# Performance work log

Measured on AMD Instinct MI355X. Metric: run time of the kernel, lower is better.

Reference implementation:

```python
import jax, jax.numpy as jnp
import numpy as np

HIDDEN = 768
NUM_EXPERTS = 8
TOP_K = 2
NUM_CLASSES = 191
Z_LOSS_COEF = 0.1
LB_COEF = 0.1
FFN = 4 * HIDDEN
EPS = 1e-5  # torch LayerNorm default


def layer_norm(x, g, b):
    m = jnp.mean(x, axis=-1, keepdims=True)
    v = jnp.mean(jnp.square(x - m), axis=-1, keepdims=True)
    return (x - m) * jax.lax.rsqrt(v + EPS) * g + b


def setup_inputs() -> dict:
    key = jax.random.key(0)
    ks = jax.random.split(key, 12)
    s = 0.02
    B, N = 256, 32
    inp = {
        'trunk_out1': jax.random.normal(ks[0], (B, N, HIDDEN), jnp.float32),
        # router: Linear -> LayerNorm -> ReLU -> (Dropout, eval) -> Linear
        'rw1': jax.random.normal(ks[1], (HIDDEN, HIDDEN), jnp.float32) * s,
        'rb1': jnp.zeros((HIDDEN,), jnp.float32),
        'rlg': jnp.ones((HIDDEN,), jnp.float32),
        'rlb': jnp.zeros((HIDDEN,), jnp.float32),
        'rw2': jax.random.normal(ks[2], (HIDDEN, NUM_EXPERTS), jnp.float32) * s,
        'rb2': jnp.zeros((NUM_EXPERTS,), jnp.float32),
        # stacked expert params [E, ...]
        'ew1': jax.random.normal(ks[3], (NUM_EXPERTS, HIDDEN, FFN), jnp.float32) * s,
        'eb1': jnp.zeros((NUM_EXPERTS, FFN), jnp.float32),
        'el1g': jnp.ones((NUM_EXPERTS, FFN), jnp.float32),
        'el1b': jnp.zeros((NUM_EXPERTS, FFN), jnp.float32),
        'ew2': jax.random.normal(ks[4], (NUM_EXPERTS, FFN, HIDDEN), jnp.float32) * s,
        'eb2': jnp.zeros((NUM_EXPERTS, HIDDEN), jnp.float32),
        'el2g': jnp.ones((NUM_EXPERTS, HIDDEN), jnp.float32),
        'el2b': jnp.zeros((NUM_EXPERTS, HIDDEN), jnp.float32),
        'ew3': jax.random.normal(ks[5], (NUM_EXPERTS, HIDDEN, NUM_CLASSES), jnp.float32) * s,
        'eb3': jnp.zeros((NUM_EXPERTS, NUM_CLASSES), jnp.float32),
    }
    return inp


def reference(trunk_out1, rw1, rb1, rlg, rlb, rw2, rb2,
              ew1, eb1, el1g, el1b, ew2, eb2, el2g, el2b, ew3, eb3):
    B, N, D = trunk_out1.shape
    x = trunk_out1.reshape(-1, D)  # [T, D], T = B*N
    T = x.shape[0]

    # router (dropout is identity in eval)
    h = jax.nn.relu(layer_norm(x @ rw1 + rb1, rlg, rlb))
    logits = h @ rw2 + rb2  # [T, E]
    probs = jax.nn.softmax(logits, axis=-1)

    topk_vals, topk_idx = jax.lax.top_k(probs, TOP_K)
    topk_vals = topk_vals / jnp.sum(topk_vals, axis=-1, keepdims=True)
    rows = jnp.arange(T)[:, None]
    mask = jnp.zeros_like(probs).at[rows, topk_idx].set(topk_vals)  # [T, E]

    z_loss = Z_LOSS_COEF * jnp.mean(jnp.square(jax.nn.logsumexp(logits, axis=-1)))
    load = jnp.mean(mask, axis=0)
    lb_loss = LB_COEF * jnp.sum(jnp.square(load - 1.0 / NUM_EXPERTS))
    aux_loss = z_loss + lb_loss

    # per-expert FFN; weighting by mask (0 for unselected) matches the
    # gather -> FFN -> weighted scatter-add of the original.
    final_logits = jnp.zeros((T, NUM_CLASSES), x.dtype)
    for e in range(NUM_EXPERTS):
        h1 = jax.nn.relu(layer_norm(x @ ew1[e] + eb1[e], el1g, el1b := el1b) if False else layer_norm(x @ ew1[e] + eb1[e], el1g[e], el1b[e]))
        h1 = jax.nn.relu(layer_norm(x @ ew1[e] + eb1[e], el1g[e], el1b[e]))  # [T, 4D]
        h2 = jax.nn.relu(layer_norm(h1 @ ew2[e] + eb2[e], el2g[e], el2b[e]))  # [T, D]
        out_e = h2 @ ew3[e] + eb3[e]  # [T, C]
        final_logits = final_logits + out_e * mask[:, e:e + 1]

    final_logits = final_logits.reshape(B, N, NUM_CLASSES).mean(axis=1)
    return final_logits, aux_loss
```

## Files before the change

### kernel.cpp

```cpp
#include <hip/hip_runtime.h>
#include <hip/hip_bf16.h>
#include <stdint.h>

#define T_TOK   8192
#define D_HID   768
#define NE      8
#define FFN_DIM 3072
#define NCLS    191
#define NSEQ    32
#define NSLOT   (T_TOK * 2)
#define NSLOTP  (NSLOT + 128)
#define LN_EPS  1e-5f
#define OUT_N   (256 * NCLS)

typedef __bf16 bf16x8 __attribute__((ext_vector_type(8)));
typedef float  f32x4  __attribute__((ext_vector_type(4)));

static __device__ __forceinline__ float bf2f(unsigned short u) {
    return __uint_as_float(((unsigned)u) << 16);
}
static __device__ __forceinline__ unsigned short f2bf(float f) {
    return __builtin_bit_cast(unsigned short, (__bf16)f);
}
static __device__ __forceinline__ float bfround(float f) {
    return (float)((__bf16)f);
}

__global__ void k_zero(float* __restrict__ out, unsigned* __restrict__ counts,
                       unsigned* __restrict__ cursors, float* __restrict__ zsum,
                       float* __restrict__ loadsum) {
    int i = blockIdx.x * 256 + threadIdx.x;
    if (i < OUT_N + 1) out[i] = 0.0f;
    if (i < NE) { counts[i] = 0u; cursors[i] = 0u; loadsum[i] = 0.0f; }
    if (i == 0) zsum[0] = 0.0f;
}

__global__ __launch_bounds__(256) void k_prep(
    const float* __restrict__ X, const float* __restrict__ RW1, const float* __restrict__ EW3,
    unsigned short* __restrict__ Xb, unsigned short* __restrict__ RW1h,
    unsigned short* __restrict__ RW1l, unsigned short* __restrict__ W3h,
    unsigned short* __restrict__ W3l) {
    const int bid = blockIdx.x, tid = threadIdx.x;
    if (bid < 3072) {
        size_t i0 = (size_t)bid * 2048 + (size_t)tid * 8;
        float4 a = *reinterpret_cast<const float4*>(X + i0);
        float4 b = *reinterpret_cast<const float4*>(X + i0 + 4);
        unsigned short t[8] = {f2bf(a.x), f2bf(a.y), f2bf(a.z), f2bf(a.w),
                               f2bf(b.x), f2bf(b.y), f2bf(b.z), f2bf(b.w)};
        *reinterpret_cast<uint4*>(Xb + i0) = *reinterpret_cast<uint4*>(t);
        return;
    }
    __shared__ float tile[64][65];
    const int rr = tid >> 2, c4 = (tid & 3) * 16;
    if (bid < 3216) {
        int t = bid - 3072, kt = t / 12, nt = t % 12;
        const float* src = RW1 + (size_t)(kt * 64 + rr) * D_HID + nt * 64 + c4;
        #pragma unroll
        for (int q = 0; q < 4; ++q) {
            float4 v = *reinterpret_cast<const float4*>(src + q * 4);
            tile[rr][c4 + q * 4 + 0] = v.x; tile[rr][c4 + q * 4 + 1] = v.y;
            tile[rr][c4 + q * 4 + 2] = v.z; tile[rr][c4 + q * 4 + 3] = v.w;
        }
        __syncthreads();
        unsigned short th[16], tl[16];
        #pragma unroll
        for (int j = 0; j < 16; ++j) {
            float f = tile[c4 + j][rr];
            th[j] = f2bf(f); tl[j] = f2bf(f - bfround(f));
        }
        size_t o = (size_t)(nt * 64 + rr) * D_HID + kt * 64 + c4;
        *reinterpret_cast<uint4*>(RW1h + o)     = *reinterpret_cast<uint4*>(&th[0]);
        *reinterpret_cast<uint4*>(RW1h + o + 8) = *reinterpret_cast<uint4*>(&th[8]);
        *reinterpret_cast<uint4*>(RW1l + o)     = *reinterpret_cast<uint4*>(&tl[0]);
        *reinterpret_cast<uint4*>(RW1l + o + 8) = *reinterpret_cast<uint4*>(&tl[8]);
    } else {
        int t = bid - 3216, e = t / 36, s = t % 36, kt = s / 3, ct = s % 3;
        const float* src = EW3 + (size_t)e * D_HID * NCLS + (size_t)(kt * 64 + rr) * NCLS;
        #pragma unroll
        for (int j = 0; j < 16; ++j) {
            int c = ct * 64 + c4 + j;
            tile[rr][c4 + j] = (c < NCLS) ? src[c] : 0.0f;
        }
        __syncthreads();
        unsigned short th[16], tl[16];
        #pragma unroll
        for (int j = 0; j < 16; ++j) {
            float f = tile[c4 + j][rr];
            th[j] = f2bf(f); tl[j] = f2bf(f - bfround(f));
        }
        size_t o = (size_t)(e * 192 + ct * 64 + rr) * D_HID + kt * 64 + c4;
        *reinterpret_cast<uint4*>(W3h + o)     = *reinterpret_cast<uint4*>(&th[0]);
        *reinterpret_cast<uint4*>(W3h + o + 8) = *reinterpret_cast<uint4*>(&th[8]);
        *reinterpret_cast<uint4*>(W3l + o)     = *reinterpret_cast<uint4*>(&tl[0]);
        *reinterpret_cast<uint4*>(W3l + o + 8) = *reinterpret_cast<uint4*>(&tl[8]);
    }
}

__global__ __launch_bounds__(256) void k_rgemm(
    const float* __restrict__ X, const unsigned short* __restrict__ RW1h,
    const unsigned short* __restrict__ RW1l, const float* __restrict__ bias,
    float* __restrict__ C) {
    const int bid = blockIdx.x;
    const int lid = (bid & 7) * 48 + (bid >> 3);
    const int m0 = (lid / 6) * 128, n0 = (lid % 6) * 128;
    __shared__ unsigned short Ah[128][40], Al[128][40], Bh[128][40], Bl[128][40];
    const int tid = threadIdx.x;
    const int wv = tid >> 6, ln = tid & 63;
    const int m_off = (wv >> 1) * 64, n_off = (wv & 1) * 64;
    const int lrow = ln & 15, lkg = ln >> 4;
    const int ar = tid >> 1, ac = (tid & 1) * 16;
    const float* aptr = X + (size_t)(m0 + ar) * D_HID + ac;
    const unsigned short* bph = RW1h + (size_t)(n0 + ar) * D_HID + ac;
    const unsigned short* bpl = RW1l + (size_t)(n0 + ar) * D_HID + ac;
    f32x4 acc[4][4] = {};
    for (int k0 = 0; k0 < D_HID; k0 += 32) {
        unsigned short th[16], tl[16];
        #pragma unroll
        for (int q = 0; q < 4; ++q) {
            float4 v = *reinterpret_cast<const float4*>(aptr + k0 + q * 4);
            float fv[4] = {v.x, v.y, v.z, v.w};
            #pragma unroll
            for (int j = 0; j < 4; ++j) {
                th[q * 4 + j] = f2bf(fv[j]);
                tl[q * 4 + j] = f2bf(fv[j] - bfround(fv[j]));
            }
        }
        *reinterpret_cast<uint4*>(&Ah[ar][ac])     = *reinterpret_cast<uint4*>(&th[0]);
        *reinterpret_cast<uint4*>(&Ah[ar][ac + 8]) = *reinterpret_cast<uint4*>(&th[8]);
        *reinterpret_cast<uint4*>(&Al[ar][ac])     = *reinterpret_cast<uint4*>(&tl[0]);
        *reinterpret_cast<uint4*>(&Al[ar][ac + 8]) = *reinterpret_cast<uint4*>(&tl[8]);
        *reinterpret_cast<uint4*>(&Bh[ar][ac])     = *reinterpret_cast<const uint4*>(bph + k0);
        *reinterpret_cast<uint4*>(&Bh[ar][ac + 8]) = *reinterpret_cast<const uint4*>(bph + k0 + 8);
        *reinterpret_cast<uint4*>(&Bl[ar][ac])     = *reinterpret_cast<const uint4*>(bpl + k0);
        *reinterpret_cast<uint4*>(&Bl[ar][ac + 8]) = *reinterpret_cast<const uint4*>(bpl + k0 + 8);
        __syncthreads();
        bf16x8 a_h[4], a_l[4];
        #pragma unroll
        for (int i = 0; i < 4; ++i) {
            a_h[i] = *reinterpret_cast<const bf16x8*>(&Ah[m_off + i * 16 + lrow][lkg * 8]);
            a_l[i] = *reinterpret_cast<const bf16x8*>(&Al[m_off + i * 16 + lrow][lkg * 8]);
        }
        #pragma unroll
        for (int j = 0; j < 4; ++j) {
            bf16x8 b_h = *reinterpret_cast<const bf16x8*>(&Bh[n_off + j * 16 + lrow][lkg * 8]);
            bf16x8 b_l = *reinterpret_cast<const bf16x8*>(&Bl[n_off + j * 16 + lrow][lkg * 8]);
            #pragma unroll
            for (int i = 0; i < 4; ++i) {
                acc[i][j] = __builtin_amdgcn_mfma_f32_16x16x32_bf16(a_h[i], b_h, acc[i][j], 0, 0, 0);
                acc[i][j] = __builtin_amdgcn_mfma_f32_16x16x32_bf16(a_h[i], b_l, acc[i][j], 0, 0, 0);
                acc[i][j] = __builtin_amdgcn_mfma_f32_16x16x32_bf16(a_l[i], b_h, acc[i][j], 0, 0, 0);
            }
        }
        __syncthreads();
    }
    #pragma unroll
    for (int i = 0; i < 4; ++i)
        #pragma unroll
        for (int r = 0; r < 4; ++r) {
            int row = m0 + m_off + i * 16 + lkg * 4 + r;
            float* dst = C + (size_t)row * D_HID;
            #pragma unroll
            for (int j = 0; j < 4; ++j) {
                int c = n0 + n_off + j * 16 + lrow;
                dst[c] = acc[i][j][r] + bias[c];
            }
        }
}

__global__ __launch_bounds__(256) void k_ln768_f32(
    float* __restrict__ Xb, const float* __restrict__ g, const float* __restrict__ b) {
    const int row = blockIdx.x;
    float* x = Xb + (size_t)row * D_HID;
    const int tid = threadIdx.x;
    float v0 = x[tid], v1 = x[tid + 256], v2 = x[tid + 512];
    float s = v0 + v1 + v2, s2 = v0 * v0 + v1 * v1 + v2 * v2;
    __shared__ float rs[4], rs2[4], mv[2];
    #pragma unroll
    for (int o = 32; o > 0; o >>= 1) { s += __shfl_down(s, o); s2 += __shfl_down(s2, o); }
    const int wv = tid >> 6, ln = tid & 63;
    if (ln == 0) { rs[wv] = s; rs2[wv] = s2; }
    __syncthreads();
    if (tid == 0) {
        float ts = rs[0] + rs[1] + rs[2] + rs[3];
        float ts2 = rs2[0] + rs2[1] + rs2[2] + rs2[3];
        float m = ts / D_HID;
        mv[0] = m; mv[1] = rsqrtf(ts2 / D_HID - m * m + LN_EPS);
    }
    __syncthreads();
    float m = mv[0], r = mv[1];
    x[tid]       = fmaxf((v0 - m) * r * g[tid]       + b[tid],       0.f);
    x[tid + 256] = fmaxf((v1 - m) * r * g[tid + 256] + b[tid + 256], 0.f);
    x[tid + 512] = fmaxf((v2 - m) * r * g[tid + 512] + b[tid + 512], 0.f);
}

__global__ __launch_bounds__(256) void k_ln768_bf16(
    unsigned short* __restrict__ Xb, const float* __restrict__ g, const float* __restrict__ b,
    const unsigned* __restrict__ eos, const unsigned* __restrict__ totp) {
    const int row = blockIdx.x;
    if ((unsigned)row >= *totp) return;
    const unsigned e = eos[row];
    const float* gp = g + (size_t)e * D_HID;
    const float* bp = b + (size_t)e * D_HID;
    unsigned short* x = Xb + (size_t)row * D_HID;
    const int tid = threadIdx.x;
    float f[4] = {0.f, 0.f, 0.f, 0.f};
    if (tid < 192) {
        ushort4 u = *reinterpret_cast<const ushort4*>(x + tid * 4);
        f[0] = bf2f(u.x); f[1] = bf2f(u.y); f[2] = bf2f(u.z); f[3] = bf2f(u.w);
    }
    float s = f[0] + f[1] + f[2] + f[3];
    float s2 = f[0] * f[0] + f[1] * f[1] + f[2] * f[2] + f[3] * f[3];
    __shared__ float rs[4], rs2[4], mv[2];
    #pragma unroll
    for (int o = 32; o > 0; o >>= 1) { s += __shfl_down(s, o); s2 += __shfl_down(s2, o); }
    const int wv = tid >> 6, ln = tid & 63;
    if (ln == 0) { rs[wv] = s; rs2[wv] = s2; }
    __syncthreads();
    if (tid == 0) {
        float ts = rs[0] + rs[1] + rs[2] + rs[3];
        float ts2 = rs2[0] + rs2[1] + rs2[2] + rs2[3];
        float m = ts / D_HID;
        mv[0] = m; mv[1] = rsqrtf(ts2 / D_HID - m * m + LN_EPS);
    }
    __syncthreads();
    if (tid < 192) {
        float m = mv[0], r = mv[1];
        float4 gg = *reinterpret_cast<const float4*>(gp + tid * 4);
        float4 bb = *reinterpret_cast<const float4*>(bp + tid * 4);
        ushort4 o;
        o.x = f2bf(fmaxf((f[0] - m) * r * gg.x + bb.x, 0.f));
        o.y = f2bf(fmaxf((f[1] - m) * r * gg.y + bb.y, 0.f));
        o.z = f2bf(fmaxf((f[2] - m) * r * gg.z + bb.z, 0.f));
        o.w = f2bf(fmaxf((f[3] - m) * r * gg.w + bb.w, 0.f));
        *reinterpret_cast<ushort4*>(x + tid * 4) = o;
    }
}

__global__ __launch_bounds__(256) void k_ln3072_bf16(
    unsigned short* __restrict__ Xb, const float* __restrict__ g, const float* __restrict__ b,
    const unsigned* __restrict__ eos, const unsigned* __restrict__ totp) {
    const int row = blockIdx.x;
    if ((unsigned)row >= *totp) return;
    const unsigned e = eos[row];
    const float* gp = g + (size_t)e * FFN_DIM;
    const float* bp = b + (size_t)e * FFN_DIM;
    unsigned short* x = Xb + (size_t)row * FFN_DIM;
    const int tid = threadIdx.x;
    float f[12];
    #pragma unroll
    for (int i = 0; i < 3; ++i) {
        ushort4 u = *reinterpret_cast<const ushort4*>(x + (i * 256 + tid) * 4);
        f[i * 4 + 0] = bf2f(u.x); f[i * 4 + 1] = bf2f(u.y);
        f[i * 4 + 2] = bf2f(u.z); f[i * 4 + 3] = bf2f(u.w);
    }
    float s = 0.f, s2 = 0.f;
    #pragma unroll
    for (int i = 0; i < 12; ++i) { s += f[i]; s2 += f[i] * f[i]; }
    __shared__ float rs[4], rs2[4], mv[2];
    #pragma unroll
    for (int o = 32; o > 0; o >>= 1) { s += __shfl_down(s, o); s2 += __shfl_down(s2, o); }
    const int wv = tid >> 6, ln = tid & 63;
    if (ln == 0) { rs[wv] = s; rs2[wv] = s2; }
    __syncthreads();
    if (tid == 0) {
        float ts = rs[0] + rs[1] + rs[2] + rs[3];
        float ts2 = rs2[0] + rs2[1] + rs2[2] + rs2[3];
        float m = ts / FFN_DIM;
        mv[0] = m; mv[1] = rsqrtf(ts2 / FFN_DIM - m * m + LN_EPS);
    }
    __syncthreads();
    float m = mv[0], r = mv[1];
    #pragma unroll
    for (int i = 0; i < 3; ++i) {
        int off = (i * 256 + tid) * 4;
        float4 gg = *reinterpret_cast<const float4*>(gp + off);
        float4 bb = *reinterpret_cast<const float4*>(bp + off);
        ushort4 o;
        o.x = f2bf(fmaxf((f[i * 4 + 0] - m) * r * gg.x + bb.x, 0.f));
        o.y = f2bf(fmaxf((f[i * 4 + 1] - m) * r * gg.y + bb.y, 0.f));
        o.z = f2bf(fmaxf((f[i * 4 + 2] - m) * r * gg.z + bb.z, 0.f));
        o.w = f2bf(fmaxf((f[i * 4 + 3] - m) * r * gg.w + bb.w, 0.f));
        *reinterpret_cast<ushort4*>(x + off) = o;
    }
}

__global__ __launch_bounds__(256) void k_router(
    const float* __restrict__ HR, const float* __restrict__ RW2, const float* __restrict__ RB2,
    unsigned* __restrict__ toke, float* __restrict__ tokw,
    unsigned* __restrict__ counts, float* __restrict__ zsum, float* __restrict__ loadsum) {
    const int wv = threadIdx.x >> 6, ln = threadIdx.x & 63;
    const int t = blockIdx.x * 4 + wv;
    __shared__ float part[4][64][9];
    float p[NE] = {};
    const float* hrow = HR + (size_t)t * D_HID;
    for (int k = ln; k < D_HID; k += 64) {
        float h = hrow[k];
        const float* w = RW2 + (size_t)k * NE;
        #pragma unroll
        for (int j = 0; j < NE; ++j) p[j] += h * w[j];
    }
    #pragma unroll
    for (int j = 0; j < NE; ++j) part[wv][ln][j] = p[j];
    __syncthreads();
    if (ln < NE) {
        float sj = 0.f;
        for (int l = 0; l < 64; ++l) sj += part[wv][l][ln];
        part[wv][0][ln] = sj + RB2[ln];
    }
    __syncthreads();
    if (ln == 0) {
        float lg[NE];
        #pragma unroll
        for (int j = 0; j < NE; ++j) lg[j] = part[wv][0][j];
        float mx = lg[0];
        #pragma unroll
        for (int j = 1; j < NE; ++j) mx = fmaxf(mx, lg[j]);
        float ex[NE], se = 0.f;
        #pragma unroll
        for (int j = 0; j < NE; ++j) { ex[j] = expf(lg[j] - mx); se += ex[j]; }
        float lse = logf(se) + mx;
        atomicAdd(zsum, lse * lse);
        int i0 = 0;
        #pragma unroll
        for (int j = 1; j < NE; ++j) if (ex[j] > ex[i0]) i0 = j;
        int i1 = (i0 == 0) ? 1 : 0;
        #pragma unroll
        for (int j = 0; j < NE; ++j) if (j != i0 && ex[j] > ex[i1]) i1 = j;
        float w0 = ex[i0] / (ex[i0] + ex[i1]);
        float w1 = 1.0f - w0;
        toke[t * 2 + 0] = (unsigned)i0; toke[t * 2 + 1] = (unsigned)i1;
        tokw[t * 2 + 0] = w0;           tokw[t * 2 + 1] = w1;
        atomicAdd(&counts[i0], 1u); atomicAdd(&counts[i1], 1u);
        atomicAdd(&loadsum[i0], w0); atomicAdd(&loadsum[i1], w1);
    }
}

__global__ void k_prefix(const unsigned* __restrict__ counts, unsigned* __restrict__ offs,
                         unsigned* __restrict__ cntp, unsigned* __restrict__ totp,
                         unsigned* __restrict__ tokv, unsigned* __restrict__ eosv,
                         float* __restrict__ wslot) {
    if (threadIdx.x == 0) {
        unsigned o = 0;
        for (int e = 0; e < NE; ++e) {
            unsigned c = counts[e];
            unsigned cp = (c + 15u) & ~15u;
            offs[e] = o; cntp[e] = cp;
            for (unsigned i = c; i < cp; ++i) {
                unsigned s = o + i;
                tokv[s] = 0u; eosv[s] = (unsigned)e; wslot[s] = 0.0f;
            }
            o += cp;
        }
        totp[0] = o;
    }
}

__global__ void k_scatter(const unsigned* __restrict__ toke, const float* __restrict__ tokw,
                          const unsigned* __restrict__ offs, unsigned* __restrict__ cursors,
                          unsigned* __restrict__ tokv, unsigned* __restrict__ eosv,
                          float* __restrict__ wslot) {
    int t = blockIdx.x * 256 + threadIdx.x;
    if (t >= T_TOK) return;
    #pragma unroll
    for (int k = 0; k < 2; ++k) {
        unsigned e = toke[t * 2 + k];
        unsigned slot = offs[e] + atomicAdd(&cursors[e], 1u);
        tokv[slot] = (unsigned)t;
        eosv[slot] = e;
        wslot[slot] = tokw[t * 2 + k];
    }
}

__global__ __launch_bounds__(256) void k_gemm1(
    const unsigned short* __restrict__ Xb, const float* __restrict__ EW1,
    const float* __restrict__ EB1, const unsigned* __restrict__ tokv,
    const unsigned* __restrict__ offs, const unsigned* __restrict__ cntp,
    unsigned short* __restrict__ H1) {
    const int bid = blockIdx.x;
    const int lid = (bid & 7) * 1536 + (bid >> 3);
    const int e = lid / 1536, rgrp = lid % 1536;
    const int sup = rgrp / 48, sub = rgrp % 48;
    const int m0 = (sup * 2 + sub / 24) * 128, n0 = (sub % 24) * 128;
    const unsigned cp = cntp[e];
    if ((unsigned)m0 >= cp) return;
    const unsigned base = offs[e];
    const float* __restrict__ W = EW1 + (size_t)e * D_HID * FFN_DIM;
    __shared__ unsigned short As[128][40];
    __shared__ unsigned short Bs[128][40];
    __shared__ unsigned stok[128];
    const int tid = threadIdx.x;
    if (tid < 128) {
        unsigned rr = (unsigned)(m0 + tid);
        stok[tid] = tokv[base + ((rr < cp) ? rr : (cp - 1u))];
    }
    __syncthreads();
    const int wv = tid >> 6, ln = tid & 63;
    const int m_off = (wv >> 1) * 64, n_off = (wv & 1) * 64;
    const int lrow = ln & 15, lkg = ln >> 4;
    const int ar = tid >> 1, ac = (tid & 1) * 16;
    const int bn = tid & 127, bq = tid >> 7;
    f32x4 acc[4][4] = {};
    const unsigned short* aptr = Xb + (size_t)stok[ar] * D_HID + ac;
    for (int k0 = 0; k0 < D_HID; k0 += 32) {
        *reinterpret_cast<uint4*>(&As[ar][ac])     = *reinterpret_cast<const uint4*>(aptr + k0);
        *reinterpret_cast<uint4*>(&As[ar][ac + 8]) = *reinterpret_cast<const uint4*>(aptr + k0 + 8);
        {
            const float* wsrc = W + (size_t)(k0 + bq * 16) * FFN_DIM + n0 + bn;
            unsigned short th[16];
            #pragma unroll
            for (int kk = 0; kk < 16; ++kk) th[kk] = f2bf(wsrc[(size_t)kk * FFN_DIM]);
            *reinterpret_cast<uint4*>(&Bs[bn][bq * 16])     = *reinterpret_cast<uint4*>(&th[0]);
            *reinterpret_cast<uint4*>(&Bs[bn][bq * 16 + 8]) = *reinterpret_cast<uint4*>(&th[8]);
        }
        __syncthreads();
        bf16x8 a[4];
        #pragma unroll
        for (int i = 0; i < 4; ++i)
            a[i] = *reinterpret_cast<const bf16x8*>(&As[m_off + i * 16 + lrow][lkg * 8]);
        #pragma unroll
        for (int j = 0; j < 4; ++j) {
            bf16x8 b = *reinterpret_cast<const bf16x8*>(&Bs[n_off + j * 16 + lrow][lkg * 8]);
            #pragma unroll
            for (int i = 0; i < 4; ++i)
                acc[i][j] = __builtin_amdgcn_mfma_f32_16x16x32_bf16(a[i], b, acc[i][j], 0, 0, 0);
        }
        __syncthreads();
    }
    const float* bias = EB1 + (size_t)e * FFN_DIM + n0;
    #pragma unroll
    for (int i = 0; i < 4; ++i)
        #pragma unroll
        for (int r = 0; r < 4; ++r) {
            unsigned rr = (unsigned)(m0 + m_off + i * 16 + lkg * 4 + r);
            if (rr < cp) {
                unsigned short* dst = H1 + (size_t)(base + rr) * FFN_DIM + n0;
                #pragma unroll
                for (int j = 0; j < 4; ++j) {
                    int c = n_off + j * 16 + lrow;
                    dst[c] = f2bf(acc[i][j][r] + bias[c]);
                }
            }
        }
}

__global__ __launch_bounds__(256) void k_gemm2(
    const unsigned short* __restrict__ H1, const float* __restrict__ EW2,
    const float* __restrict__ EB2, const unsigned* __restrict__ offs,
    const unsigned* __restrict__ cntp, unsigned short* __restrict__ H2b) {
    const int bid = blockIdx.x;
    const int lid = (bid & 7) * 384 + (bid >> 3);
    const int e = lid / 384, rgrp = lid % 384;
    const int m0 = (rgrp / 6) * 128, n0 = (rgrp % 6) * 128;
    const unsigned cp = cntp[e];
    if ((unsigned)m0 >= cp) return;
    const unsigned base = offs[e];
    const float* __restrict__ W = EW2 + (size_t)e * FFN_DIM * D_HID;
    __shared__ unsigned short As[128][40];
    __shared__ unsigned short Bs[128][40];
    const int tid = threadIdx.x;
    const int wv = tid >> 6, ln = tid & 63;
    const int m_off = (wv >> 1) * 64, n_off = (wv & 1) * 64;
    const int lrow = ln & 15, lkg = ln >> 4;
    const int ar = tid >> 1, ac = (tid & 1) * 16;
    const int bn = tid & 127, bq = tid >> 7;
    unsigned arow = (unsigned)(m0 + ar);
    if (arow >= cp) arow = cp - 1u;
    const unsigned short* aptr = H1 + (size_t)(base + arow) * FFN_DIM + ac;
    f32x4 acc[4][4] = {};
    for (int k0 = 0; k0 < FFN_DIM; k0 += 32) {
        *reinterpret_cast<uint4*>(&As[ar][ac])     = *reinterpret_cast<const uint4*>(aptr + k0);
        *reinterpret_cast<uint4*>(&As[ar][ac + 8]) = *reinterpret_cast<const uint4*>(aptr + k0 + 8);
        {
            const float* wsrc = W + (size_t)(k0 + bq * 16) * D_HID + n0 + bn;
            unsigned short th[16];
            #pragma unroll
            for (int kk = 0; kk < 16; ++kk) th[kk] = f2bf(wsrc[(size_t)kk * D_HID]);
            *reinterpret_cast<uint4*>(&Bs[bn][bq * 16])     = *reinterpret_cast<uint4*>(&th[0]);
            *reinterpret_cast<uint4*>(&Bs[bn][bq * 16 + 8]) = *reinterpret_cast<uint4*>(&th[8]);
        }
        __syncthreads();
        bf16x8 a[4];
        #pragma unroll
        for (int i = 0; i < 4; ++i)
            a[i] = *reinterpret_cast<const bf16x8*>(&As[m_off + i * 16 + lrow][lkg * 8]);
        #pragma unroll
        for (int j = 0; j < 4; ++j) {
            bf16x8 b = *reinterpret_cast<const bf16x8*>(&Bs[n_off + j * 16 + lrow][lkg * 8]);
            #pragma unroll
            for (int i = 0; i < 4; ++i)
                acc[i][j] = __builtin_amdgcn_mfma_f32_16x16x32_bf16(a[i], b, acc[i][j], 0, 0, 0);
        }
        __syncthreads();
    }
    const float* bias = EB2 + (size_t)e * D_HID + n0;
    #pragma unroll
    for (int i = 0; i < 4; ++i)
        #pragma unroll
        for (int r = 0; r < 4; ++r) {
            unsigned rr = (unsigned)(m0 + m_off + i * 16 + lkg * 4 + r);
            if (rr < cp) {
                unsigned short* dst = H2b + (size_t)(base + rr) * D_HID + n0;
                #pragma unroll
                for (int j = 0; j < 4; ++j) {
                    int c = n_off + j * 16 + lrow;
                    dst[c] = f2bf(acc[i][j][r] + bias[c]);
                }
            }
        }
}

__global__ __launch_bounds__(256) void k_gemm3(
    const unsigned short* __restrict__ H2b, const unsigned short* __restrict__ W3h,
    const unsigned short* __restrict__ W3l, const float* __restrict__ EB3,
    const unsigned* __restrict__ tokv, const unsigned* __restrict__ offs,
    const unsigned* __restrict__ cntp, const float* __restrict__ wslot,
    float* __restrict__ out) {
    const int bid = blockIdx.x;
    const int lid = (bid & 7) * 128 + (bid >> 3);
    const int e = lid >> 7, mg = lid & 127;
    const int m0 = mg * 64;
    const unsigned cp = cntp[e];
    if ((unsigned)m0 >= cp) return;
    const unsigned base = offs[e];
    __shared__ unsigned short As[64][40];
    __shared__ unsigned short Bh[192][40];
    __shared__ unsigned short Bl[192][40];
    const int tid = threadIdx.x;
    const int wv = tid >> 6, ln = tid & 63;
    const int m_off = (wv >> 1) * 32, n_off = (wv & 1) * 96;
    const int lrow = ln & 15, lkg = ln >> 4;
    const int ar = tid >> 2, ac = (tid & 3) * 8;
    unsigned arow = (unsigned)(m0 + ar);
    if (arow >= cp) arow = cp - 1u;
    const unsigned short* aptr = H2b + (size_t)(base + arow) * D_HID + ac;
    const unsigned short* w3hb = W3h + (size_t)e * 192 * D_HID;
    const unsigned short* w3lb = W3l + (size_t)e * 192 * D_HID;
    f32x4 acc[2][6] = {};
    for (int k0 = 0; k0 < D_HID; k0 += 32) {
        *reinterpret_cast<uint4*>(&As[ar][ac]) = *reinterpret_cast<const uint4*>(aptr + k0);
        #pragma unroll
        for (int q = 0; q < 3; ++q) {
            int task = tid + q * 256;
            int br = task >> 2, bs = (task & 3) * 8;
            *reinterpret_cast<uint4*>(&Bh[br][bs]) =
                *reinterpret_cast<const uint4*>(w3hb + (size_t)br * D_HID + k0 + bs);
            *reinterpret_cast<uint4*>(&Bl[br][bs]) =
                *reinterpret_cast<const uint4*>(w3lb + (size_t)br * D_HID + k0 + bs);
        }
        __syncthreads();
        bf16x8 a0 = *reinterpret_cast<const bf16x8*>(&As[m_off + lrow][lkg * 8]);
        bf16x8 a1 = *reinterpret_cast<const bf16x8*>(&As[m_off + 16 + lrow][lkg * 8]);
        #pragma unroll
        for (int j = 0; j < 6; ++j) {
            bf16x8 bh = *reinterpret_cast<const bf16x8*>(&Bh[n_off + j * 16 + lrow][lkg * 8]);
            bf16x8 bl = *reinterpret_cast<const bf16x8*>(&Bl[n_off + j * 16 + lrow][lkg * 8]);
            acc[0][j] = __builtin_amdgcn_mfma_f32_16x16x32_bf16(a0, bh, acc[0][j], 0, 0, 0);
            acc[0][j] = __builtin_amdgcn_mfma_f32_16x16x32_bf16(a0, bl, acc[0][j], 0, 0, 0);
            acc[1][j] = __builtin_amdgcn_mfma_f32_16x16x32_bf16(a1, bh, acc[1][j], 0, 0, 0);
            acc[1][j] = __builtin_amdgcn_mfma_f32_16x16x32_bf16(a1, bl, acc[1][j], 0, 0, 0);
        }
        __syncthreads();
    }
    const float* b3 = EB3 + (size_t)e * NCLS;
    #pragma unroll
    for (int i = 0; i < 2; ++i)
        #pragma unroll
        for (int r = 0; r < 4; ++r) {
            unsigned rr = (unsigned)(m0 + m_off + i * 16 + lkg * 4 + r);
            if (rr < cp) {
                unsigned slot = base + rr;
                float w = wslot[slot] * (1.0f / NSEQ);
                if (w != 0.0f) {
                    unsigned bno = tokv[slot] >> 5;
                    float* op = out + (size_t)bno * NCLS;
                    #pragma unroll
                    for (int j = 0; j < 6; ++j) {
                        int c = n_off + j * 16 + lrow;
                        if (c < NCLS) atomicAdd(op + c, w * (acc[i][j][r] + b3[c]));
                    }
                }
            }
        }
}

__global__ void k_aux(const float* __restrict__ zsum, const float* __restrict__ loadsum,
                      float* __restrict__ out) {
    if (threadIdx.x == 0) {
        float z = 0.1f * zsum[0] / (float)T_TOK;
        float lb = 0.f;
        for (int e = 0; e < NE; ++e) {
            float d = loadsum[e] / (float)T_TOK - 0.125f;
            lb += d * d;
        }
        out[OUT_N] = z + 0.1f * lb;
    }
}

extern "C" void kernel_launch(void* const* d_in, const int* in_sizes, int n_in,
                              void* d_out, int out_size, void* d_ws, size_t ws_size,
                              hipStream_t stream) {
    (void)in_sizes; (void)n_in; (void)out_size; (void)ws_size;
    const float* x    = (const float*)d_in[0];
    const float* rw1  = (const float*)d_in[1];
    const float* rb1  = (const float*)d_in[2];
    const float* rlg  = (const float*)d_in[3];
    const float* rlb  = (const float*)d_in[4];
    const float* rw2  = (const float*)d_in[5];
    const float* rb2  = (const float*)d_in[6];
    const float* ew1  = (const float*)d_in[7];
    const float* eb1  = (const float*)d_in[8];
    const float* el1g = (const float*)d_in[9];
    const float* el1b = (const float*)d_in[10];
    const float* ew2  = (const float*)d_in[11];
    const float* eb2  = (const float*)d_in[12];
    const float* el2g = (const float*)d_in[13];
    const float* el2b = (const float*)d_in[14];
    const float* ew3  = (const float*)d_in[15];
    const float* eb3  = (const float*)d_in[16];
    float* out = (float*)d_out;

    uint8_t* ws = (uint8_t*)d_ws;
    float* hr            = (float*)ws;
    unsigned short* h2b  = (unsigned short*)ws;
    size_t off = 25362432;
    unsigned short* rw1h = (unsigned short*)(ws + off); off += 1179648;
    unsigned short* rw1l = (unsigned short*)(ws + off); off += 1179648;
    unsigned short* xb   = (unsigned short*)(ws + off); off += 12582912;
    unsigned short* w3h  = (unsigned short*)(ws + off); off += 2359296;
    unsigned short* w3l  = (unsigned short*)(ws + off); off += 2359296;
    unsigned short* h1   = (unsigned short*)(ws + off); off += 101449728;
    uint8_t* sb = ws + off;
    unsigned* tokv    = (unsigned*)sb;
    unsigned* eosv    = tokv + NSLOTP;
    float*    wslot   = (float*)(eosv + NSLOTP);
    unsigned* toke    = (unsigned*)(wslot + NSLOTP);
    float*    tokw    = (float*)(toke + NSLOT);
    unsigned* counts  = (unsigned*)(tokw + NSLOT);
    unsigned* cursors = counts + NE;
    unsigned* offs    = cursors + NE;
    unsigned* cntp    = offs + NE;
    unsigned* totp    = cntp + NE;
    float*    zsum    = (float*)(totp + 1);
    float*    loadsum = zsum + 1;

    k_zero<<<dim3(192), dim3(256), 0, stream>>>(out, counts, cursors, zsum, loadsum);
    k_prep<<<dim3(3504), dim3(256), 0, stream>>>(x, rw1, ew3, xb, rw1h, rw1l, w3h, w3l);
    k_rgemm<<<dim3(384), dim3(256), 0, stream>>>(x, rw1h, rw1l, rb1, hr);
    k_ln768_f32<<<dim3(T_TOK), dim3(256), 0, stream>>>(hr, rlg, rlb);
    k_router<<<dim3(T_TOK / 4), dim3(256), 0, stream>>>(
        hr, rw2, rb2, toke, tokw, counts, zsum, loadsum);
    k_prefix<<<dim3(1), dim3(64), 0, stream>>>(counts, offs, cntp, totp, tokv, eosv, wslot);
    k_scatter<<<dim3(T_TOK / 256), dim3(256), 0, stream>>>(
        toke, tokw, offs, cursors, tokv, eosv, wslot);
    k_gemm1<<<dim3(12288), dim3(256), 0, stream>>>(xb, ew1, eb1, tokv, offs, cntp, h1);
    k_ln3072_bf16<<<dim3(NSLOTP), dim3(256), 0, stream>>>(h1, el1g, el1b, eosv, totp);
    k_gemm2<<<dim3(3072), dim3(256), 0, stream>>>(h1, ew2, eb2, offs, cntp, h2b);
    k_ln768_bf16<<<dim3(NSLOTP), dim3(256), 0, stream>>>(h2b, el2g, el2b, eosv, totp);
    k_gemm3<<<dim3(1024), dim3(256), 0, stream>>>(
        h2b, w3h, w3l, eb3, tokv, offs, cntp, wslot, out);
    k_aux<<<dim3(1), dim3(64), 0, stream>>>(zsum, loadsum, out);
}
```

Measured before the change: 1.412 ms.

## Pre-convert expert FFN weights to transposed bf16 in prep kernel

Adds prep blocks that transpose and convert the ew1 and ew2 expert weights to bf16 once per call. The expert GEMMs can then load B tiles as contiguous 16-byte vectors instead of doing strided fp32 loads and converting inside every tile. The block-to-tile mapping also changes so that experts are interleaved and M tiles are grouped differently for better weight reuse in L2. This costs extra workspace and an extra pass over 75 MB of weights each call, and the new path is only taken when the workspace is large enough.

```diff
diff --git a/kernel.cpp b/kernel.cpp
--- a/kernel.cpp
+++ b/kernel.cpp
@@ -37,9 +37,11 @@
 
 __global__ __launch_bounds__(256) void k_prep(
     const float* __restrict__ X, const float* __restrict__ RW1, const float* __restrict__ EW3,
+    const float* __restrict__ EW1, const float* __restrict__ EW2,
     unsigned short* __restrict__ Xb, unsigned short* __restrict__ RW1h,
     unsigned short* __restrict__ RW1l, unsigned short* __restrict__ W3h,
-    unsigned short* __restrict__ W3l) {
+    unsigned short* __restrict__ W3l, unsigned short* __restrict__ EW1B,
+    unsigned short* __restrict__ EW2B) {
     const int bid = blockIdx.x, tid = threadIdx.x;
     if (bid < 3072) {
         size_t i0 = (size_t)bid * 2048 + (size_t)tid * 8;
@@ -73,7 +75,7 @@
         *reinterpret_cast<uint4*>(RW1h + o + 8) = *reinterpret_cast<uint4*>(&th[8]);
         *reinterpret_cast<uint4*>(RW1l + o)     = *reinterpret_cast<uint4*>(&tl[0]);
         *reinterpret_cast<uint4*>(RW1l + o + 8) = *reinterpret_cast<uint4*>(&tl[8]);
-    } else {
+    } else if (bid < 3504) {
         int t = bid - 3216, e = t / 36, s = t % 36, kt = s / 3, ct = s % 3;
         const float* src = EW3 + (size_t)e * D_HID * NCLS + (size_t)(kt * 64 + rr) * NCLS;
         #pragma unroll
@@ -93,6 +95,38 @@
         *reinterpret_cast<uint4*>(W3h + o + 8) = *reinterpret_cast<uint4*>(&th[8]);
         *reinterpret_cast<uint4*>(W3l + o)     = *reinterpret_cast<uint4*>(&tl[0]);
         *reinterpret_cast<uint4*>(W3l + o + 8) = *reinterpret_cast<uint4*>(&tl[8]);
+    } else if (bid < 8112) {
+        int t = bid - 3504, e = t / 576, s = t % 576, kt = s / 48, nt = s % 48;
+        const float* src = EW1 + (size_t)e * D_HID * FFN_DIM + (size_t)(kt * 64 + rr) * FFN_DIM + nt * 64 + c4;
+        #pragma unroll
+        for (int q = 0; q < 4; ++q) {
+            float4 v = *reinterpret_cast<const float4*>(src + q * 4);
+            tile[rr][c4 + q * 4 + 0] = v.x; tile[rr][c4 + q * 4 + 1] = v.y;
+            tile[rr][c4 + q * 4 + 2] = v.z; tile[rr][c4 + q * 4 + 3] = v.w;
+        }
+        __syncthreads();
+        unsigned short th[16];
+        #pragma unroll
+        for (int j = 0; j < 16; ++j) th[j] = f2bf(tile[c4 + j][rr]);
+        size_t o = (size_t)e * FFN_DIM * D_HID + (size_t)(nt * 64 + rr) * D_HID + kt * 64 + c4;
+        *reinterpret_cast<uint4*>(EW1B + o)     = *reinterpret_cast<uint4*>(&th[0]);
+        *reinterpret_cast<uint4*>(EW1B + o + 8) = *reinterpret_cast<uint4*>(&th[8]);
+    } else {
+        int t = bid - 8112, e = t / 576, s = t % 576, kt = s / 12, nt = s % 12;
+        const float* src = EW2 + (size_t)e * FFN_DIM * D_HID + (size_t)(kt * 64 + rr) * D_HID + nt * 64 + c4;
+        #pragma unroll
+        for (int q = 0; q < 4; ++q) {
+            float4 v = *reinterpret_cast<const float4*>(src + q * 4);
+            tile[rr][c4 + q * 4 + 0] = v.x; tile[rr][c4 + q * 4 + 1] = v.y;
+            tile[rr][c4 + q * 4 + 2] = v.z; tile[rr][c4 + q * 4 + 3] = v.w;
+        }
+        __syncthreads();
+        unsigned short th[16];
+        #pragma unroll
+        for (int j = 0; j < 16; ++j) th[j] = f2bf(tile[c4 + j][rr]);
+        size_t o = (size_t)e * D_HID * FFN_DIM + (size_t)(nt * 64 + rr) * FFN_DIM + kt * 64 + c4;
+        *reinterpret_cast<uint4*>(EW2B + o)     = *reinterpret_cast<uint4*>(&th[0]);
+        *reinterpret_cast<uint4*>(EW2B + o + 8) = *reinterpret_cast<uint4*>(&th[8]);
     }
 }
 
@@ -371,20 +405,18 @@
     }
 }
 
+template<bool CVT>
 __global__ __launch_bounds__(256) void k_gemm1(
     const unsigned short* __restrict__ Xb, const float* __restrict__ EW1,
-    const float* __restrict__ EB1, const unsigned* __restrict__ tokv,
-    const unsigned* __restrict__ offs, const unsigned* __restrict__ cntp,
-    unsigned short* __restrict__ H1) {
+    const unsigned short* __restrict__ EW1B, const float* __restrict__ EB1,
+    const unsigned* __restrict__ tokv, const unsigned* __restrict__ offs,
+    const unsigned* __restrict__ cntp, unsigned short* __restrict__ H1) {
     const int bid = blockIdx.x;
-    const int lid = (bid & 7) * 1536 + (bid >> 3);
-    const int e = lid / 1536, rgrp = lid % 1536;
-    const int sup = rgrp / 48, sub = rgrp % 48;
-    const int m0 = (sup * 2 + sub / 24) * 128, n0 = (sub % 24) * 128;
+    const int e = bid & 7, rgrp = bid >> 3;
+    const int n0 = (rgrp >> 6) * 128, m0 = (rgrp & 63) * 128;
     const unsigned cp = cntp[e];
     if ((unsigned)m0 >= cp) return;
     const unsigned base = offs[e];
-    const float* __restrict__ W = EW1 + (size_t)e * D_HID * FFN_DIM;
     __shared__ unsigned short As[128][40];
     __shared__ unsigned short Bs[128][40];
     __shared__ unsigned stok[128];
@@ -401,11 +433,16 @@
     const int bn = tid & 127, bq = tid >> 7;
     f32x4 acc[4][4] = {};
     const unsigned short* aptr = Xb + (size_t)stok[ar] * D_HID + ac;
+    const unsigned short* bptr = EW1B + ((size_t)e * FFN_DIM + n0 + ar) * D_HID + ac;
+    const float* wsrc0 = EW1 + (size_t)e * D_HID * FFN_DIM + (size_t)(bq * 16) * FFN_DIM + n0 + bn;
     for (int k0 = 0; k0 < D_HID; k0 += 32) {
         *reinterpret_cast<uint4*>(&As[ar][ac])     = *reinterpret_cast<const uint4*>(aptr + k0);
         *reinterpret_cast<uint4*>(&As[ar][ac + 8]) = *reinterpret_cast<const uint4*>(aptr + k0 + 8);
-        {
-            const float* wsrc = W + (size_t)(k0 + bq * 16) * FFN_DIM + n0 + bn;
+        if (CVT) {
+            *reinterpret_cast<uint4*>(&Bs[ar][ac])     = *reinterpret_cast<const uint4*>(bptr + k0);
+            *reinterpret_cast<uint4*>(&Bs[ar][ac + 8]) = *reinterpret_cast<const uint4*>(bptr + k0 + 8);
+        } else {
+            const float* wsrc = wsrc0 + (size_t)k0 * FFN_DIM;
             unsigned short th[16];
             #pragma unroll
             for (int kk = 0; kk < 16; ++kk) th[kk] = f2bf(wsrc[(size_t)kk * FFN_DIM]);
@@ -443,18 +480,19 @@
         }
 }
 
+template<bool CVT>
 __global__ __launch_bounds__(256) void k_gemm2(
     const unsigned short* __restrict__ H1, const float* __restrict__ EW2,
-    const float* __restrict__ EB2, const unsigned* __restrict__ offs,
-    const unsigned* __restrict__ cntp, unsigned short* __restrict__ H2b) {
+    const unsigned short* __restrict__ EW2B, const float* __restrict__ EB2,
+    const unsigned* __restrict__ offs, const unsigned* __restrict__ cntp,
+    unsigned short* __restrict__ H2b) {
     const int bid = blockIdx.x;
-    const int lid = (bid & 7) * 384 + (bid >> 3);
-    const int e = lid / 384, rgrp = lid % 384;
-    const int m0 = (rgrp / 6) * 128, n0 = (rgrp % 6) * 128;
+    const int e = bid & 7, rgrp = bid >> 3;
+    const int slab = rgrp / 48, w = rgrp % 48;
+    const int m0 = (slab * 8 + (w & 7)) * 128, n0 = (w >> 3) * 128;
     const unsigned cp = cntp[e];
     if ((unsigned)m0 >= cp) return;
     const unsigned base = offs[e];
-    const float* __restrict__ W = EW2 + (size_t)e * FFN_DIM * D_HID;
     __shared__ unsigned short As[128][40];
     __shared__ unsigned short Bs[128][40];
     const int tid = threadIdx.x;
@@ -466,12 +504,17 @@
     unsigned arow = (unsigned)(m0 + ar);
     if (arow >= cp) arow = cp - 1u;
     const unsigned short* aptr = H1 + (size_t)(base + arow) * FFN_DIM + ac;
+    const unsigned short* bptr = EW2B + ((size_t)e * D_HID + n0 + ar) * FFN_DIM + ac;
+    const float* wsrc0 = EW2 + (size_t)e * FFN_DIM * D_HID + (size_t)(bq * 16) * D_HID + n0 + bn;
     f32x4 acc[4][4] = {};
     for (int k0 = 0; k0 < FFN_DIM; k0 += 32) {
         *reinterpret_cast<uint4*>(&As[ar][ac])     = *reinterpret_cast<const uint4*>(aptr + k0);
         *reinterpret_cast<uint4*>(&As[ar][ac + 8]) = *reinterpret_cast<const uint4*>(aptr + k0 + 8);
-        {
-            const float* wsrc = W + (size_t)(k0 + bq * 16) * D_HID + n0 + bn;
+        if (CVT) {
+            *reinterpret_cast<uint4*>(&Bs[ar][ac])     = *reinterpret_cast<const uint4*>(bptr + k0);
+            *reinterpret_cast<uint4*>(&Bs[ar][ac + 8]) = *reinterpret_cast<const uint4*>(bptr + k0 + 8);
+        } else {
+            const float* wsrc = wsrc0 + (size_t)k0 * D_HID;
             unsigned short th[16];
             #pragma unroll
             for (int kk = 0; kk < 16; ++kk) th[kk] = f2bf(wsrc[(size_t)kk * D_HID]);
@@ -599,7 +642,7 @@
 extern "C" void kernel_launch(void* const* d_in, const int* in_sizes, int n_in,
                               void* d_out, int out_size, void* d_ws, size_t ws_size,
                               hipStream_t stream) {
-    (void)in_sizes; (void)n_in; (void)out_size; (void)ws_size;
+    (void)in_sizes; (void)n_in; (void)out_size;
     const float* x    = (const float*)d_in[0];
     const float* rw1  = (const float*)d_in[1];
     const float* rb1  = (const float*)d_in[2];
@@ -628,6 +671,14 @@
     unsigned short* xb   = (unsigned short*)(ws + off); off += 12582912;
     unsigned short* w3h  = (unsigned short*)(ws + off); off += 2359296;
     unsigned short* w3l  = (unsigned short*)(ws + off); off += 2359296;
+    const size_t need_cvt = off + 75497472ull + 101449728ull + 400000ull;
+    const bool cvt = ws_size >= need_cvt;
+    unsigned short* ew1b = nullptr;
+    unsigned short* ew2b = nullptr;
+    if (cvt) {
+        ew1b = (unsigned short*)(ws + off); off += 37748736;
+        ew2b = (unsigned short*)(ws + off); off += 37748736;
+    }
     unsigned short* h1   = (unsigned short*)(ws + off); off += 101449728;
     uint8_t* sb = ws + off;
     unsigned* tokv    = (unsigned*)sb;
@@ -644,7 +695,8 @@
     float*    loadsum = zsum + 1;
 
     k_zero<<<dim3(192), dim3(256), 0, stream>>>(out, counts, cursors, zsum, loadsum);
-    k_prep<<<dim3(3504), dim3(256), 0, stream>>>(x, rw1, ew3, xb, rw1h, rw1l, w3h, w3l);
+    k_prep<<<dim3(cvt ? 12720 : 3504), dim3(256), 0, stream>>>(
+        x, rw1, ew3, ew1, ew2, xb, rw1h, rw1l, w3h, w3l, ew1b, ew2b);
     k_rgemm<<<dim3(384), dim3(256), 0, stream>>>(x, rw1h, rw1l, rb1, hr);
     k_ln768_f32<<<dim3(T_TOK), dim3(256), 0, stream>>>(hr, rlg, rlb);
     k_router<<<dim3(T_TOK / 4), dim3(256), 0, stream>>>(
@@ -652,9 +704,21 @@
     k_prefix<<<dim3(1), dim3(64), 0, stream>>>(counts, offs, cntp, totp, tokv, eosv, wslot);
     k_scatter<<<dim3(T_TOK / 256), dim3(256), 0, stream>>>(
         toke, tokw, offs, cursors, tokv, eosv, wslot);
-    k_gemm1<<<dim3(12288), dim3(256), 0, stream>>>(xb, ew1, eb1, tokv, offs, cntp, h1);
+    if (cvt) {
+        k_gemm1<true><<<dim3(12288), dim3(256), 0, stream>>>(
+            xb, ew1, ew1b, eb1, tokv, offs, cntp, h1);
+    } else {
+        k_gemm1<false><<<dim3(12288), dim3(256), 0, stream>>>(
+            xb, ew1, ew1b, eb1, tokv, offs, cntp, h1);
+    }
     k_ln3072_bf16<<<dim3(NSLOTP), dim3(256), 0, stream>>>(h1, el1g, el1b, eosv, totp);
-    k_gemm2<<<dim3(3072), dim3(256), 0, stream>>>(h1, ew2, eb2, offs, cntp, h2b);
+    if (cvt) {
+        k_gemm2<true><<<dim3(3072), dim3(256), 0, stream>>>(
+            h1, ew2, ew2b, eb2, offs, cntp, h2b);
+    } else {
+        k_gemm2<false><<<dim3(3072), dim3(256), 0, stream>>>(
+            h1, ew2, ew2b, eb2, offs, cntp, h2b);
+    }
     k_ln768_bf16<<<dim3(NSLOTP), dim3(256), 0, stream>>>(h2b, el2g, el2b, eosv, totp);
     k_gemm3<<<dim3(1024), dim3(256), 0, stream>>>(
         h2b, w3h, w3l, eb3, tokv, offs, cntp, wslot, out);
```

Measured after the change: 1.383 ms. -2.0%, faster.
